# Kernel tuning notes

Measured on AMD Instinct MI355X. Metric: run time of the kernel, lower is better.

## Reference

```python
import jax, jax.numpy as jnp
import numpy as np

INIT_STD = 0.002
DEFAULT_BETA = 1.0 / np.sqrt(64.0)  # 1/sqrt(head_dim)


def setup_inputs() -> dict:
    key = jax.random.key(0)
    k1, k2, k3 = jax.random.split(key, 3)
    B, S, E = 4, 2048, 768
    H, D = 12, 64
    x = jax.random.normal(k1, (B, S, E), dtype=jnp.float32)
    q_proj_weight = INIT_STD * jax.random.normal(k2, (H, D, E), dtype=jnp.float32)
    k_proj_weight = INIT_STD * jax.random.normal(k3, (H, D, E), dtype=jnp.float32)
    beta = jnp.full((H,), DEFAULT_BETA, dtype=jnp.float32)
    return {"x": x, "q_proj_weight": q_proj_weight, "k_proj_weight": k_proj_weight, "beta": beta}


def reference(x, q_proj_weight, k_proj_weight, beta):
    # x: [B,S,E]; W^{Q,K}: [H,D,E]; beta: [H]
    q = jnp.einsum("bse,hde->bshd", x, q_proj_weight)  # [B,S,H,D]
    k = jnp.einsum("bse,hde->bshd", x, k_proj_weight)  # [B,S,H,D]
    # scores[b,h,s,t] = beta_h * <Q_{bsh}, K_{bth}>
    scores = jnp.einsum("bshd,bthd,h->bhst", q, k, beta)
    S = x.shape[1]
    diag = jnp.eye(S, dtype=bool)  # self-exclusion mask (B != C)
    scores = jnp.where(diag[None, None, :, :], -jnp.inf, scores)
    lse = jax.nn.logsumexp(scores, axis=-1)  # [B,H,S]
    # E = -sum_{b,h,s} (1/beta_h) * logsumexp_t
    energy = -jnp.sum(lse / beta[None, :, None])
    return energy
```

## Files before the change

kernel.cpp:

```cpp
#include <hip/hip_runtime.h>
#include <hip/hip_bf16.h>

typedef __attribute__((ext_vector_type(8))) short short8v;
typedef __attribute__((ext_vector_type(4))) float f32x4;

static constexpr int B_ = 4, S_ = 2048, E_ = 768, H_ = 12, D_ = 64;
static constexpr int NROWS = B_ * H_ * S_;
static constexpr float LOG2E = 1.44269504088896340736f;
static constexpr float LN2 = 0.69314718055994530942f;

typedef __attribute__((address_space(3))) unsigned int lds_u32;
typedef const __attribute__((address_space(1))) unsigned int glb_u32;

__device__ __forceinline__ void gload16(const void* g, void* l) {
  __builtin_amdgcn_global_load_lds((glb_u32*)g, (lds_u32*)l, 16, 0, 0);
}

#define VM0 asm volatile("s_waitcnt vmcnt(0)" ::: "memory")
#define VM2 asm volatile("s_waitcnt vmcnt(2)" ::: "memory")
#define VM4 asm volatile("s_waitcnt vmcnt(4)" ::: "memory")
#define LG0 asm volatile("s_waitcnt lgkmcnt(0)" ::: "memory")
#define BAR __builtin_amdgcn_s_barrier()

__device__ __forceinline__ unsigned short f2bf(float f) {
  union { float f; unsigned int u; } v; v.f = f;
  unsigned int u = v.u;
  unsigned int r = (u + 0x7fffu + ((u >> 16) & 1u)) >> 16;
  return (unsigned short)r;
}

__global__ __launch_bounds__(256) void cvt_w_kernel(const float4* __restrict__ wq,
                                                    const float4* __restrict__ wk,
                                                    const float* __restrict__ beta,
                                                    ushort4* __restrict__ wb, int n4) {
  int i = blockIdx.x * 256 + threadIdx.x;
  if (i < n4) {
    int row = i / (E_ / 4);
    float sc = beta[row >> 6] * LOG2E;
    float4 v = wq[i];
    ushort4 o;
    o.x = f2bf(v.x * sc); o.y = f2bf(v.y * sc); o.z = f2bf(v.z * sc); o.w = f2bf(v.w * sc);
    wb[i] = o;
  } else if (i < 2 * n4) {
    int j = i - n4;
    float4 v = wk[j];
    ushort4 o;
    o.x = f2bf(v.x); o.y = f2bf(v.y); o.z = f2bf(v.z); o.w = f2bf(v.w);
    wb[i] = o;
  }
}

__global__ __launch_bounds__(256) void proj_kernel(const float* __restrict__ x,
                                                   const unsigned short* __restrict__ wb,
                                                   unsigned short* __restrict__ Qb,
                                                   unsigned short* __restrict__ Kb) {
  __shared__ unsigned short lA[128 * 32];
  __shared__ unsigned short lB[128 * 32];
  const int mt = blockIdx.x, nt = blockIdx.y;
  const int t = threadIdx.x;
  const int wid = t >> 6, lane = t & 63, l15 = lane & 15, lhi = lane >> 4;
  const int wr = (wid >> 1) * 64, wc = (wid & 1) * 64;

  f32x4 acc[4][4] = {};

  const int row = t >> 2, ch = t & 3;
  const int chs = ch ^ (row & 3);
  const float* gA = x + (size_t)(mt * 128 + row) * E_ + chs * 8;
  const unsigned short* gB = wb + (size_t)(nt * 128 + row) * E_ + chs * 8;

  f32x4 a0 = *(const f32x4*)(gA);
  f32x4 a1 = *(const f32x4*)(gA + 4);
  f32x4 a2 = *(const f32x4*)(gA + 64 * E_);
  f32x4 a3 = *(const f32x4*)(gA + 64 * E_ + 4);

  for (int k0 = 0; k0 < E_; k0 += 32) {
    BAR;
    gload16(gB + k0, &lB[t * 8]);
    gload16(gB + (size_t)64 * E_ + k0, &lB[2048 + t * 8]);
    VM2;
    union { short8v s8; unsigned int u[4]; } c0, c1;
    asm("v_cvt_pk_bf16_f32 %0, %1, %2" : "=v"(c0.u[0]) : "v"(a0[0]), "v"(a0[1]));
    asm("v_cvt_pk_bf16_f32 %0, %1, %2" : "=v"(c0.u[1]) : "v"(a0[2]), "v"(a0[3]));
    asm("v_cvt_pk_bf16_f32 %0, %1, %2" : "=v"(c0.u[2]) : "v"(a1[0]), "v"(a1[1]));
    asm("v_cvt_pk_bf16_f32 %0, %1, %2" : "=v"(c0.u[3]) : "v"(a1[2]), "v"(a1[3]));
    asm("v_cvt_pk_bf16_f32 %0, %1, %2" : "=v"(c1.u[0]) : "v"(a2[0]), "v"(a2[1]));
    asm("v_cvt_pk_bf16_f32 %0, %1, %2" : "=v"(c1.u[1]) : "v"(a2[2]), "v"(a2[3]));
    asm("v_cvt_pk_bf16_f32 %0, %1, %2" : "=v"(c1.u[2]) : "v"(a3[0]), "v"(a3[1]));
    asm("v_cvt_pk_bf16_f32 %0, %1, %2" : "=v"(c1.u[3]) : "v"(a3[2]), "v"(a3[3]));
    *(short8v*)&lA[row * 32 + ch * 8] = c0.s8;
    *(short8v*)&lA[(row + 64) * 32 + ch * 8] = c1.s8;
    if (k0 + 32 < E_) {
      a0 = *(const f32x4*)(gA + k0 + 32);
      a1 = *(const f32x4*)(gA + k0 + 36);
      a2 = *(const f32x4*)(gA + 64 * E_ + k0 + 32);
      a3 = *(const f32x4*)(gA + 64 * E_ + k0 + 36);
      LG0;
      VM4;
    } else {
      LG0;
      VM0;
    }
    BAR;
    short8v aF[4], bF[4];
#pragma unroll
    for (int m = 0; m < 4; ++m) {
      const int r = wr + m * 16 + l15;
      aF[m] = *(const short8v*)&lA[r * 32 + ((lhi ^ (l15 & 3)) << 3)];
    }
#pragma unroll
    for (int n = 0; n < 4; ++n) {
      const int r = wc + n * 16 + l15;
      bF[n] = *(const short8v*)&lB[r * 32 + ((lhi ^ (l15 & 3)) << 3)];
    }
#pragma unroll
    for (int m = 0; m < 4; ++m)
#pragma unroll
      for (int n = 0; n < 4; ++n)
        acc[m][n] = __builtin_amdgcn_mfma_f32_16x16x32_bf16(aF[m], bF[n], acc[m][n], 0, 0, 0);
  }

  const int nbase = nt * 128 + wc;
  unsigned short* dst = (nbase < 768) ? Qb : Kb;
  const int nb = (nbase < 768) ? nbase : nbase - 768;
#pragma unroll
  for (int m = 0; m < 4; ++m)
#pragma unroll
    for (int n = 0; n < 4; ++n)
#pragma unroll
      for (int r = 0; r < 4; ++r) {
        int M = mt * 128 + wr + m * 16 + lhi * 4 + r;
        int col = nb + n * 16 + l15;
        int h = col >> 6, d = col & 63;
        int b = M >> 11, s = M & (S_ - 1);
        dst[((((size_t)b * H_ + h) * S_ + s) << 6) + d] = f2bf(acc[m][n][r]);
      }
}

__device__ __forceinline__ void stageK(const unsigned short* __restrict__ Kbase, int t0,
                                       int tid, unsigned short* lbuf) {
  const int w = tid >> 6;
  const int r = tid >> 3;
  const int c = (tid & 7) ^ (r & 7);
  const char* src = (const char*)Kbase + ((size_t)(t0 + r) << 7) + (c << 4);
  char* ldst = (char*)lbuf + (w << 10);
  gload16(src, ldst);
  gload16(src + (32 << 7), ldst + 4096);
}

__device__ __forceinline__ void computeTile64(const unsigned short* lbuf, const short8v q[4][2],
                                              f32x4 sp[4], bool isD, int l15, int lhi) {
  short8v kf[4][2];
  const int sw = l15 & 7;
#pragma unroll
  for (int f = 0; f < 4; ++f) {
    const char* p = (const char*)lbuf + ((f * 16 + l15) << 7);
    kf[f][0] = *(const short8v*)(p + ((lhi ^ sw) << 4));
    kf[f][1] = *(const short8v*)(p + (((lhi + 4) ^ sw) << 4));
  }
#pragma unroll
  for (int rb = 0; rb < 4; ++rb) {
    f32x4 acc[4] = {};
#pragma unroll
    for (int f = 0; f < 4; ++f) {
      acc[f] = __builtin_amdgcn_mfma_f32_16x16x32_bf16(q[rb][0], kf[f][0], acc[f], 0, 0, 0);
      acc[f] = __builtin_amdgcn_mfma_f32_16x16x32_bf16(q[rb][1], kf[f][1], acc[f], 0, 0, 0);
    }
#pragma unroll
    for (int f = 0; f < 4; ++f) {
      f32x4 e;
#pragma unroll
      for (int r = 0; r < 4; ++r) e[r] = __builtin_amdgcn_exp2f(acc[f][r]);
      if (isD && f == rb) {
#pragma unroll
        for (int r = 0; r < 4; ++r)
          if (l15 == lhi * 4 + r) e[r] = 0.f;
      }
      sp[rb] += e;
    }
  }
}

__global__ __launch_bounds__(256) void lse_kernel(const unsigned short* __restrict__ Qb,
                                                  const unsigned short* __restrict__ Kb,
                                                  float* __restrict__ rowsum) {
  __shared__ __align__(16) unsigned short lK[3][4096];
  const int L = blockIdx.x + 8 * (blockIdx.y + 12 * blockIdx.z);
  const int xcd = L & 7, j = L >> 3;
  const int split = j & 3;
  const int st = (j >> 2) & 7;
  const int g = xcd + 8 * (j >> 5);
  const int h = g % H_, b = g / H_;

  const int tid = threadIdx.x;
  const int wid = tid >> 6, lane = tid & 63;
  const int l15 = lane & 15, lhi = lane >> 4;
  const size_t hb = ((size_t)b * H_ + h) * S_;
  const unsigned short* Qbase = Qb + hb * D_;
  const unsigned short* Kbase = Kb + hb * D_;
  const int s0 = st * 256 + wid * 64;
  const int tb = split * 512;

  short8v q[4][2];
#pragma unroll
  for (int rb = 0; rb < 4; ++rb) {
    const unsigned short* qr = Qbase + (size_t)(s0 + rb * 16 + l15) * D_ + lhi * 8;
    q[rb][0] = *(const short8v*)qr;
    q[rb][1] = *(const short8v*)(qr + 32);
  }

  const int dtile = ((s0 >> 9) == split) ? ((s0 - tb) >> 6) : -1;

  f32x4 sp[4] = {};
  stageK(Kbase, tb, tid, lK[0]);
  stageK(Kbase, tb + 64, tid, lK[1]);
  int bi = 0;
#pragma unroll 1
  for (int i = 0; i < 7; ++i) {
    VM2;
    BAR;
    if (i < 6) {
      int bs_ = bi + 2; if (bs_ >= 3) bs_ -= 3;
      stageK(Kbase, tb + (i + 2) * 64, tid, lK[bs_]);
    }
    computeTile64(lK[bi], q, sp, i == dtile, l15, lhi);
    if (++bi == 3) bi = 0;
  }
  VM0; BAR;
  computeTile64(lK[bi], q, sp, 7 == dtile, l15, lhi);

#pragma unroll
  for (int rb = 0; rb < 4; ++rb)
#pragma unroll
    for (int r = 0; r < 4; ++r) {
      float s = sp[rb][r];
#pragma unroll
      for (int off = 1; off < 16; off <<= 1) s += __shfl_xor(s, off, 64);
      if (l15 == 0)
        rowsum[(size_t)split * NROWS + hb + s0 + rb * 16 + lhi * 4 + r] = s;
    }
}

__global__ __launch_bounds__(256) void finish1_kernel(const float* __restrict__ rowsum,
                                                      const float* __restrict__ beta,
                                                      float* __restrict__ partial) {
  int row = blockIdx.x * 256 + threadIdx.x;
  float s = (rowsum[row] + rowsum[NROWS + row]) +
            (rowsum[2 * NROWS + row] + rowsum[3 * NROWS + row]);
  int h = (row >> 11) % H_;
  float c = __builtin_amdgcn_logf(s) * LN2 / beta[h];
#pragma unroll
  for (int off = 1; off < 64; off <<= 1) c += __shfl_xor(c, off, 64);
  __shared__ float wsum[4];
  int wid = threadIdx.x >> 6;
  if ((threadIdx.x & 63) == 0) wsum[wid] = c;
  __syncthreads();
  if (threadIdx.x == 0) partial[blockIdx.x] = wsum[0] + wsum[1] + wsum[2] + wsum[3];
}

__global__ __launch_bounds__(256) void finish2_kernel(const float* __restrict__ partial, int n,
                                                      float* __restrict__ out) {
  float s = 0.f;
  for (int i = threadIdx.x; i < n; i += 256) s += partial[i];
#pragma unroll
  for (int off = 1; off < 64; off <<= 1) s += __shfl_xor(s, off, 64);
  __shared__ float wsum[4];
  int wid = threadIdx.x >> 6;
  if ((threadIdx.x & 63) == 0) wsum[wid] = s;
  __syncthreads();
  if (threadIdx.x == 0) out[0] = -(wsum[0] + wsum[1] + wsum[2] + wsum[3]);
}

extern "C" void kernel_launch(void* const* d_in, const int* in_sizes, int n_in,
                              void* d_out, int out_size, void* d_ws, size_t ws_size,
                              hipStream_t stream) {
  const float* x    = (const float*)d_in[0];
  const float* wq   = (const float*)d_in[1];
  const float* wk   = (const float*)d_in[2];
  const float* beta = (const float*)d_in[3];

  char* ws = (char*)d_ws;
  const size_t wb_bytes = (size_t)2 * H_ * D_ * E_ * 2;
  const size_t qk_bytes = (size_t)B_ * H_ * S_ * D_ * 2;
  const size_t rs_bytes = (size_t)4 * NROWS * 4;
  unsigned short* wb = (unsigned short*)ws;
  unsigned short* Qb = (unsigned short*)(ws + wb_bytes);
  unsigned short* Kb = (unsigned short*)(ws + wb_bytes + qk_bytes);
  float* rowsum      = (float*)(ws + wb_bytes + 2 * qk_bytes);
  float* partial     = (float*)(ws + wb_bytes + 2 * qk_bytes + rs_bytes);

  int nw4 = (H_ * D_ * E_) / 4;
  cvt_w_kernel<<<(2 * nw4 + 255) / 256, 256, 0, stream>>>((const float4*)wq, (const float4*)wk,
                                                          beta, (ushort4*)wb, nw4);

  dim3 pgrid((B_ * S_) / 128, (2 * H_ * D_) / 128);
  proj_kernel<<<pgrid, 256, 0, stream>>>(x, wb, Qb, Kb);

  dim3 lgrid(S_ / 256, H_, B_ * 4);
  lse_kernel<<<lgrid, 256, 0, stream>>>(Qb, Kb, rowsum);

  finish1_kernel<<<NROWS / 256, 256, 0, stream>>>(rowsum, beta, partial);
  finish2_kernel<<<1, 256, 0, stream>>>(partial, NROWS / 256, (float*)d_out);
}
```

Measured before the change: 76.28 us.

## Multi-buffer LDS tiles in projection GEMM to prefetch ahead, one barrier

The projection GEMM now double-buffers the converted x tile in LDS and triple-buffers the bf16 weight tile, issuing weight loads two K-steps ahead. The main loop drops from two barriers per K-step to one, and the wait on the weight tile becomes vmcnt(2) so the next tile's load can stay in flight. This is meant to hide global-load latency behind the MFMA work. It costs extra LDS per block, which may lower occupancy.

```diff
diff --git a/kernel.cpp b/kernel.cpp
--- a/kernel.cpp
+++ b/kernel.cpp
@@ -18,7 +18,6 @@
 
 #define VM0 asm volatile("s_waitcnt vmcnt(0)" ::: "memory")
 #define VM2 asm volatile("s_waitcnt vmcnt(2)" ::: "memory")
-#define VM4 asm volatile("s_waitcnt vmcnt(4)" ::: "memory")
 #define LG0 asm volatile("s_waitcnt lgkmcnt(0)" ::: "memory")
 #define BAR __builtin_amdgcn_s_barrier()
 
@@ -54,8 +53,8 @@
                                                    const unsigned short* __restrict__ wb,
                                                    unsigned short* __restrict__ Qb,
                                                    unsigned short* __restrict__ Kb) {
-  __shared__ unsigned short lA[128 * 32];
-  __shared__ unsigned short lB[128 * 32];
+  __shared__ unsigned short lA[2][128 * 32];
+  __shared__ unsigned short lB[3][128 * 32];
   const int mt = blockIdx.x, nt = blockIdx.y;
   const int t = threadIdx.x;
   const int wid = t >> 6, lane = t & 63, l15 = lane & 15, lhi = lane >> 4;
@@ -72,12 +71,16 @@
   f32x4 a1 = *(const f32x4*)(gA + 4);
   f32x4 a2 = *(const f32x4*)(gA + 64 * E_);
   f32x4 a3 = *(const f32x4*)(gA + 64 * E_ + 4);
-
-  for (int k0 = 0; k0 < E_; k0 += 32) {
-    BAR;
-    gload16(gB + k0, &lB[t * 8]);
-    gload16(gB + (size_t)64 * E_ + k0, &lB[2048 + t * 8]);
-    VM2;
+  gload16(gB, &lB[0][t * 8]);
+  gload16(gB + (size_t)64 * E_, &lB[0][2048 + t * 8]);
+  gload16(gB + 32, &lB[1][t * 8]);
+  gload16(gB + (size_t)64 * E_ + 32, &lB[1][2048 + t * 8]);
+
+  int cb = 0, sb = 2;
+#pragma unroll 1
+  for (int i = 0; i < 24; ++i) {
+    const int k0 = i * 32;
+    if (i == 23) { VM0; } else { VM2; }
     union { short8v s8; unsigned int u[4]; } c0, c1;
     asm("v_cvt_pk_bf16_f32 %0, %1, %2" : "=v"(c0.u[0]) : "v"(a0[0]), "v"(a0[1]));
     asm("v_cvt_pk_bf16_f32 %0, %1, %2" : "=v"(c0.u[1]) : "v"(a0[2]), "v"(a0[3]));
@@ -87,36 +90,40 @@
     asm("v_cvt_pk_bf16_f32 %0, %1, %2" : "=v"(c1.u[1]) : "v"(a2[2]), "v"(a2[3]));
     asm("v_cvt_pk_bf16_f32 %0, %1, %2" : "=v"(c1.u[2]) : "v"(a3[0]), "v"(a3[1]));
     asm("v_cvt_pk_bf16_f32 %0, %1, %2" : "=v"(c1.u[3]) : "v"(a3[2]), "v"(a3[3]));
-    *(short8v*)&lA[row * 32 + ch * 8] = c0.s8;
-    *(short8v*)&lA[(row + 64) * 32 + ch * 8] = c1.s8;
-    if (k0 + 32 < E_) {
+    *(short8v*)&lA[i & 1][row * 32 + ch * 8] = c0.s8;
+    *(short8v*)&lA[i & 1][(row + 64) * 32 + ch * 8] = c1.s8;
+    LG0;
+    BAR;
+    if (i < 23) {
       a0 = *(const f32x4*)(gA + k0 + 32);
       a1 = *(const f32x4*)(gA + k0 + 36);
       a2 = *(const f32x4*)(gA + 64 * E_ + k0 + 32);
       a3 = *(const f32x4*)(gA + 64 * E_ + k0 + 36);
-      LG0;
-      VM4;
-    } else {
-      LG0;
-      VM0;
-    }
-    BAR;
+    }
+    if (i < 22) {
+      gload16(gB + k0 + 64, &lB[sb][t * 8]);
+      gload16(gB + (size_t)64 * E_ + k0 + 64, &lB[sb][2048 + t * 8]);
+    }
     short8v aF[4], bF[4];
+    const unsigned short* pa = lA[i & 1];
+    const unsigned short* pb = lB[cb];
 #pragma unroll
     for (int m = 0; m < 4; ++m) {
       const int r = wr + m * 16 + l15;
-      aF[m] = *(const short8v*)&lA[r * 32 + ((lhi ^ (l15 & 3)) << 3)];
+      aF[m] = *(const short8v*)&pa[r * 32 + ((lhi ^ (l15 & 3)) << 3)];
     }
 #pragma unroll
     for (int n = 0; n < 4; ++n) {
       const int r = wc + n * 16 + l15;
-      bF[n] = *(const short8v*)&lB[r * 32 + ((lhi ^ (l15 & 3)) << 3)];
+      bF[n] = *(const short8v*)&pb[r * 32 + ((lhi ^ (l15 & 3)) << 3)];
     }
 #pragma unroll
     for (int m = 0; m < 4; ++m)
 #pragma unroll
       for (int n = 0; n < 4; ++n)
         acc[m][n] = __builtin_amdgcn_mfma_f32_16x16x32_bf16(aF[m], bF[n], acc[m][n], 0, 0, 0);
+    cb = (cb == 2) ? 0 : cb + 1;
+    sb = (sb == 2) ? 0 : sb + 1;
   }
 
   const int nbase = nt * 128 + wc;
```

Result: slower. 78.52 us (+2.9%).
